# Performance work log

Measured on AMD Instinct MI355X. Metric: run time of the kernel, lower is better.

Reference implementation:

```python
import jax, jax.numpy as jnp
import numpy as np

D_MODEL = 1024
HIDDEN = 4096
N_EXPERTS = 8
TOP_K = 2


def setup_inputs() -> dict:
    key = jax.random.key(0)
    k_x, k_r, k_w1, k_w2 = jax.random.split(key, 4)
    x = jax.random.normal(k_x, (2, 1024, D_MODEL), dtype=jnp.float32)
    # router: nn.Linear(d_model, n_experts, bias=False) -> weight [E, D]; store transposed [D, E]
    Wr = jax.random.normal(k_r, (D_MODEL, N_EXPERTS), dtype=jnp.float32) * 0.02
    # expert w1: Linear(D, H) -> store [E, D, H]; w2: Linear(H, D) -> [E, H, D]
    W1 = jax.random.normal(k_w1, (N_EXPERTS, D_MODEL, HIDDEN), dtype=jnp.float32) * 0.02
    W2 = jax.random.normal(k_w2, (N_EXPERTS, HIDDEN, D_MODEL), dtype=jnp.float32) * 0.02
    return {"x": x, "Wr": Wr, "W1": W1, "W2": W2}


def reference(x, Wr, W1, W2):
    B, S, D = x.shape
    flat = x.reshape(-1, D)                       # [T, D]
    logits = flat @ Wr                            # [T, E]
    top_vals, top_idx = jax.lax.top_k(logits, TOP_K)
    # softmax over the top-k logits; forward only uses slot 0 (faithful to source)
    weights = jax.nn.softmax(top_vals, axis=-1)   # [T, K]
    top1 = top_idx[:, 0]                          # [T] int
    w_top1 = weights[:, 0]                        # [T]
    # dense all-expert compute (fixed small E loop fused into batched einsum)
    h = jax.nn.gelu(jnp.einsum('td,edh->teh', flat, W1), approximate=False)  # [T,E,H]
    y = jnp.einsum('teh,ehd->ted', h, W2)         # [T, E, D]
    y_sel = jnp.take_along_axis(y, top1[:, None, None], axis=1)[:, 0, :]     # [T, D]
    out = (w_top1[:, None] * y_sel).reshape(B, S, D)
    return out
```

## Files before the change

### kernel.cpp

```cpp
#include <hip/hip_runtime.h>
#include <math.h>

#define T_TOKENS 2048
#define DMODEL   1024
#define HID      4096
#define NEXP     8
#define MAX_TILES 32

typedef float  f32x4  __attribute__((ext_vector_type(4)));
typedef short  bf16x8 __attribute__((ext_vector_type(8)));

__device__ __forceinline__ unsigned short f2bf(float f) {
    union { float f; unsigned u; } v; v.f = f;
    unsigned u = v.u;
    unsigned r = (u + 0x7FFFu + ((u >> 16) & 1u)) >> 16;
    return (unsigned short)r;
}

__device__ __forceinline__ unsigned pk2bf(float lo, float hi) {
    unsigned r;
    asm("v_cvt_pk_bf16_f32 %0, %1, %2" : "=v"(r) : "v"(lo), "v"(hi));
    return r;
}

__device__ __forceinline__ float f4get(const float4& v, int i) {
    return i == 0 ? v.x : i == 1 ? v.y : i == 2 ? v.z : v.w;
}

__device__ __forceinline__ void async_copy16(const void* g, void* l) {
    __builtin_amdgcn_global_load_lds(
        (const __attribute__((address_space(1))) void*)g,
        (__attribute__((address_space(3))) void*)l,
        16, 0, 0);
}

__global__ __launch_bounds__(64) void router_kernel(
    const float* __restrict__ x, const float* __restrict__ Wr,
    int* counts, int* expert_of, int* slot_of, float* wt_of,
    unsigned short* __restrict__ Xbf) {
    int t = blockIdx.x;
    int lane = threadIdx.x;
    const float* xr = x + (size_t)t * DMODEL;
    unsigned short* xb = Xbf + (size_t)t * DMODEL;
    float p[NEXP];
#pragma unroll
    for (int e = 0; e < NEXP; ++e) p[e] = 0.f;
#pragma unroll
    for (int q = 0; q < 4; ++q) {
        int d = q * 256 + lane * 4;
        float4 v = *(const float4*)(xr + d);
        ushort4 b;
        b.x = f2bf(v.x); b.y = f2bf(v.y); b.z = f2bf(v.z); b.w = f2bf(v.w);
        *(ushort4*)(xb + d) = b;
#pragma unroll
        for (int j = 0; j < 4; ++j) {
            float xv = f4get(v, j);
            const float* wr = Wr + (size_t)(d + j) * NEXP;
#pragma unroll
            for (int e = 0; e < NEXP; ++e) p[e] += xv * wr[e];
        }
    }
#pragma unroll
    for (int e = 0; e < NEXP; ++e) {
        for (int off = 32; off > 0; off >>= 1)
            p[e] += __shfl_down(p[e], off, 64);
    }
    if (lane == 0) {
        int i0 = 0; float v0 = p[0];
        for (int e = 1; e < NEXP; ++e) if (p[e] > v0) { v0 = p[e]; i0 = e; }
        float v1 = -INFINITY;
        for (int e = 0; e < NEXP; ++e) if (e != i0 && p[e] > v1) v1 = p[e];
        float w = 1.f / (1.f + expf(v1 - v0));
        expert_of[t] = i0;
        wt_of[t] = w;
        slot_of[t] = atomicAdd(&counts[i0], 1);
    }
}

__global__ void scan_scatter_kernel(const int* counts, int* offsets,
                                    int* tileE, int* tileM, int* tileCount,
                                    const int* expert_of, const int* slot_of,
                                    int* perm) {
    __shared__ int soff[NEXP];
    if (threadIdx.x == 0) {
        int run = 0, tc = 0;
        for (int e = 0; e < NEXP; ++e) {
            offsets[e] = run; soff[e] = run;
            for (int m0 = 0; m0 < counts[e]; m0 += 128) {
                tileE[tc] = e; tileM[tc] = m0; ++tc;
            }
            run += counts[e];
        }
        *tileCount = tc;
    }
    __syncthreads();
    for (int t = threadIdx.x; t < T_TOKENS; t += blockDim.x)
        perm[soff[expert_of[t]] + slot_of[t]] = t;
}

__global__ __launch_bounds__(256, 2) void gemm1_kernel(
    const unsigned short* __restrict__ Xbf, const float* __restrict__ W1,
    const int* __restrict__ counts, const int* __restrict__ offsets,
    const int* __restrict__ perm, const int* __restrict__ tileE,
    const int* __restrict__ tileM, const int* __restrict__ tileCount,
    unsigned short* __restrict__ H) {

    const int NT = HID / 128;
    int tile = blockIdx.x / NT;
    int nt   = blockIdx.x % NT;
    if (tile >= *tileCount) return;
    int e = tileE[tile], m0 = tileM[tile];
    int rows_e = counts[e], base = offsets[e];
    int n0 = nt * 128;

    __shared__ unsigned short Alds[2][128 * 64];
    __shared__ unsigned short Blds[2][128 * 64];

    int tid  = threadIdx.x;
    int lane = tid & 63;
    int wid  = tid >> 6;
    int wm = wid >> 1, wn = wid & 1;
    const int swz = (lane & 7) << 4;

    const unsigned short* ag[4];
    int aoff[4];
#pragma unroll
    for (int p = 0; p < 4; ++p) {
        int idx = p * 256 + tid;
        int row = idx >> 3;
        int seg = (idx & 7) ^ (row & 7);
        int r = m0 + row;
        int tok = perm[base + (r < rows_e ? r : rows_e - 1)];
        ag[p] = Xbf + (size_t)tok * DMODEL + seg * 8;
        aoff[p] = idx * 16;
    }

    const int kq4 = (tid & 15) * 4;
    const int nb  = (tid >> 4) * 8;
    const float* bsrc = W1 + ((size_t)e * DMODEL + kq4) * HID + n0 + nb;
    float4 breg[8];

    f32x4 acc[4][4];
#pragma unroll
    for (int i = 0; i < 4; ++i)
#pragma unroll
        for (int j = 0; j < 4; ++j) acc[i][j] = (f32x4){0.f, 0.f, 0.f, 0.f};

#define G_ISSUE(kt, BUF, STRIDE) do {                                         \
    _Pragma("unroll")                                                         \
    for (int r_ = 0; r_ < 4; ++r_) {                                          \
        _Pragma("unroll")                                                     \
        for (int q_ = 0; q_ < 2; ++q_)                                        \
            breg[r_*2+q_] = *(const float4*)(bsrc + ((size_t)(kt)*64 + r_) * (STRIDE) + q_*4); \
    }                                                                         \
    _Pragma("unroll")                                                         \
    for (int p_ = 0; p_ < 4; ++p_)                                            \
        async_copy16(ag[p_] + (kt) * 64, (char*)Alds[BUF] + aoff[p_]);        \
} while (0)

#define G_WRITEB(BUF) do {                                                    \
    char* bb_ = (char*)Blds[BUF];                                             \
    _Pragma("unroll")                                                         \
    for (int j_ = 0; j_ < 8; ++j_) {                                          \
        unsigned lo_ = pk2bf(f4get(breg[0 + (j_>>2)], j_&3),                  \
                             f4get(breg[2 + (j_>>2)], j_&3));                 \
        unsigned hi_ = pk2bf(f4get(breg[4 + (j_>>2)], j_&3),                  \
                             f4get(breg[6 + (j_>>2)], j_&3));                 \
        unsigned long long w_ = ((unsigned long long)hi_ << 32) | lo_;        \
        *(unsigned long long*)(bb_ + (nb + j_) * 128 + ((kq4 * 2) ^ (j_ << 4))) = w_; \
    }                                                                         \
} while (0)

#define G_COMPUTE(BUF) do {                                                   \
    const char* ab_ = (const char*)Alds[BUF];                                 \
    const char* bb_ = (const char*)Blds[BUF];                                 \
    _Pragma("unroll")                                                         \
    for (int ks_ = 0; ks_ < 2; ++ks_) {                                       \
        int kb_ = (ks_ * 32 + ((lane >> 4) * 8)) * 2;                         \
        bf16x8 af_[4], bf_[4];                                                \
        _Pragma("unroll")                                                     \
        for (int i_ = 0; i_ < 4; ++i_) {                                      \
            int m_ = wm * 64 + i_ * 16 + (lane & 15);                         \
            af_[i_] = *(const bf16x8*)(ab_ + m_ * 128 + (kb_ ^ swz));         \
            int n_ = wn * 64 + i_ * 16 + (lane & 15);                         \
            bf_[i_] = *(const bf16x8*)(bb_ + n_ * 128 + (kb_ ^ swz));         \
        }                                                                     \
        _Pragma("unroll")                                                     \
        for (int i_ = 0; i_ < 4; ++i_)                                        \
            _Pragma("unroll")                                                 \
            for (int j_ = 0; j_ < 4; ++j_)                                    \
                acc[i_][j_] = __builtin_amdgcn_mfma_f32_16x16x32_bf16(af_[i_], bf_[j_], acc[i_][j_], 0, 0, 0); \
    }                                                                         \
} while (0)

    G_ISSUE(0, 0, HID);
    G_WRITEB(0);
    __syncthreads();

#pragma unroll 1
    for (int t = 0; t < 16; t += 2) {
        G_ISSUE(t + 1, 1, HID);
        G_COMPUTE(0);
        G_WRITEB(1);
        __syncthreads();
        if (t + 2 < 16) G_ISSUE(t + 2, 0, HID);
        G_COMPUTE(1);
        if (t + 2 < 16) G_WRITEB(0);
        __syncthreads();
    }

    int quad = lane >> 4, col = lane & 15;
#pragma unroll
    for (int i = 0; i < 4; ++i)
#pragma unroll
        for (int j = 0; j < 4; ++j)
#pragma unroll
            for (int r = 0; r < 4; ++r) {
                int ml = wm * 64 + i * 16 + quad * 4 + r;
                if (m0 + ml < rows_e) {
                    int n = n0 + wn * 64 + j * 16 + col;
                    float v = acc[i][j][r];
                    float g = 0.5f * v * (1.0f + erff(v * 0.70710678118654752f));
                    H[(size_t)(base + m0 + ml) * HID + n] = f2bf(g);
                }
            }
}

__global__ __launch_bounds__(256, 2) void gemm2_kernel(
    const unsigned short* __restrict__ H, const float* __restrict__ W2,
    const int* __restrict__ counts, const int* __restrict__ offsets,
    const int* __restrict__ perm, const float* __restrict__ wt_of,
    const int* __restrict__ tileE, const int* __restrict__ tileM,
    const int* __restrict__ tileCount, float* __restrict__ out) {

    const int NT = DMODEL / 128;
    const int SK = 4;
    int tile = blockIdx.x / (NT * SK);
    int rem  = blockIdx.x % (NT * SK);
    int nt   = rem >> 2;
    int sk   = rem & 3;
    if (tile >= *tileCount) return;
    int e = tileE[tile], m0 = tileM[tile];
    int rows_e = counts[e], base = offsets[e];
    int n0 = nt * 128;
    int kbeg = sk * (HID / SK);

    __shared__ unsigned short Alds[2][128 * 64];
    __shared__ unsigned short Blds[2][128 * 64];
    __shared__ int   rowTok[128];
    __shared__ float rowW[128];

    int tid  = threadIdx.x;
    int lane = tid & 63;
    int wid  = tid >> 6;
    int wm = wid >> 1, wn = wid & 1;
    const int swz = (lane & 7) << 4;

    if (tid < 128) {
        int r = m0 + tid;
        if (r < rows_e) {
            int tok = perm[base + r];
            rowTok[tid] = tok;
            rowW[tid]   = wt_of[tok];
        } else { rowTok[tid] = 0; rowW[tid] = 0.f; }
    }

    const unsigned short* ag[4];
    int aoff[4];
#pragma unroll
    for (int p = 0; p < 4; ++p) {
        int idx = p * 256 + tid;
        int row = idx >> 3;
        int seg = (idx & 7) ^ (row & 7);
        int hr = base + m0 + row;
        if (hr > T_TOKENS - 1) hr = T_TOKENS - 1;
        ag[p] = H + (size_t)hr * HID + kbeg + seg * 8;
        aoff[p] = idx * 16;
    }

    const int kq4 = (tid & 15) * 4;
    const int nb  = (tid >> 4) * 8;
    const float* bsrc = W2 + ((size_t)e * HID + kbeg + kq4) * DMODEL + n0 + nb;
    float4 breg[8];

    f32x4 acc[4][4];
#pragma unroll
    for (int i = 0; i < 4; ++i)
#pragma unroll
        for (int j = 0; j < 4; ++j) acc[i][j] = (f32x4){0.f, 0.f, 0.f, 0.f};

    G_ISSUE(0, 0, DMODEL);
    G_WRITEB(0);
    __syncthreads();

#pragma unroll 1
    for (int t = 0; t < 16; t += 2) {
        G_ISSUE(t + 1, 1, DMODEL);
        G_COMPUTE(0);
        G_WRITEB(1);
        __syncthreads();
        if (t + 2 < 16) G_ISSUE(t + 2, 0, DMODEL);
        G_COMPUTE(1);
        if (t + 2 < 16) G_WRITEB(0);
        __syncthreads();
    }

    int quad = lane >> 4, col = lane & 15;
#pragma unroll
    for (int i = 0; i < 4; ++i)
#pragma unroll
        for (int j = 0; j < 4; ++j)
#pragma unroll
            for (int r = 0; r < 4; ++r) {
                int ml = wm * 64 + i * 16 + quad * 4 + r;
                if (m0 + ml < rows_e) {
                    int tok = rowTok[ml];
                    float w = rowW[ml];
                    int n = n0 + wn * 64 + j * 16 + col;
                    atomicAdd(&out[(size_t)tok * DMODEL + n], w * acc[i][j][r]);
                }
            }
}

extern "C" void kernel_launch(void* const* d_in, const int* in_sizes, int n_in,
                              void* d_out, int out_size, void* d_ws, size_t ws_size,
                              hipStream_t stream) {
    const float* x  = (const float*)d_in[0];
    const float* Wr = (const float*)d_in[1];
    const float* W1 = (const float*)d_in[2];
    const float* W2 = (const float*)d_in[3];
    float* out = (float*)d_out;

    char* ws = (char*)d_ws;
    int*   counts    = (int*)(ws);
    int*   offsets   = (int*)(ws + 64);
    int*   tileCount = (int*)(ws + 128);
    int*   tileE     = (int*)(ws + 256);
    int*   tileM     = (int*)(ws + 256 + 4 * MAX_TILES);
    int*   expert_of = (int*)(ws + 1024);
    int*   slot_of   = (int*)(ws + 1024 + 8192);
    float* wt_of     = (float*)(ws + 1024 + 16384);
    int*   perm      = (int*)(ws + 1024 + 24576);
    size_t off = 65536;
    unsigned short* Xbf  = (unsigned short*)(ws + off); off += (size_t)T_TOKENS * DMODEL * 2;
    unsigned short* Hbuf = (unsigned short*)(ws + off);

    hipMemsetAsync(counts, 0, 64, stream);
    hipMemsetAsync(out, 0, (size_t)T_TOKENS * DMODEL * sizeof(float), stream);

    router_kernel<<<T_TOKENS, 64, 0, stream>>>(x, Wr, counts, expert_of, slot_of, wt_of, Xbf);
    scan_scatter_kernel<<<1, 256, 0, stream>>>(counts, offsets, tileE, tileM, tileCount,
                                               expert_of, slot_of, perm);

    gemm1_kernel<<<MAX_TILES * (HID / 128), 256, 0, stream>>>(
        Xbf, W1, counts, offsets, perm, tileE, tileM, tileCount, Hbuf);
    gemm2_kernel<<<MAX_TILES * (DMODEL / 128) * 4, 256, 0, stream>>>(
        Hbuf, W2, counts, offsets, perm, wt_of, tileE, tileM, tileCount, out);
}
```

Before: 438.2 us.

## Double threads per GEMM block and register-prefetch A/B tiles two stages ahead

```diff
diff --git a/kernel.cpp b/kernel.cpp
--- a/kernel.cpp
+++ b/kernel.cpp
@@ -27,19 +27,21 @@
     return i == 0 ? v.x : i == 1 ? v.y : i == 2 ? v.z : v.w;
 }
 
-__device__ __forceinline__ void async_copy16(const void* g, void* l) {
-    __builtin_amdgcn_global_load_lds(
-        (const __attribute__((address_space(1))) void*)g,
-        (__attribute__((address_space(3))) void*)l,
-        16, 0, 0);
-}
-
-__global__ __launch_bounds__(64) void router_kernel(
+#define SBAR() __builtin_amdgcn_sched_barrier(0)
+
+__device__ __forceinline__ void barrier_lds() {
+    asm volatile("s_waitcnt lgkmcnt(0)" ::: "memory");
+    SBAR();
+    __builtin_amdgcn_s_barrier();
+    SBAR();
+}
+
+__global__ __launch_bounds__(256) void router_kernel(
     const float* __restrict__ x, const float* __restrict__ Wr,
     int* counts, int* expert_of, int* slot_of, float* wt_of,
     unsigned short* __restrict__ Xbf) {
-    int t = blockIdx.x;
-    int lane = threadIdx.x;
+    int lane = threadIdx.x & 63;
+    int t = blockIdx.x * 4 + (threadIdx.x >> 6);
     const float* xr = x + (size_t)t * DMODEL;
     unsigned short* xb = Xbf + (size_t)t * DMODEL;
     float p[NEXP];
@@ -98,7 +100,7 @@
         perm[soff[expert_of[t]] + slot_of[t]] = t;
 }
 
-__global__ __launch_bounds__(256, 2) void gemm1_kernel(
+__global__ __launch_bounds__(512, 4) void gemm1_kernel(
     const unsigned short* __restrict__ Xbf, const float* __restrict__ W1,
     const int* __restrict__ counts, const int* __restrict__ offsets,
     const int* __restrict__ perm, const int* __restrict__ tileE,
@@ -122,101 +124,103 @@
     int wm = wid >> 1, wn = wid & 1;
     const int swz = (lane & 7) << 4;
 
-    const unsigned short* ag[4];
-    int aoff[4];
-#pragma unroll
-    for (int p = 0; p < 4; ++p) {
-        int idx = p * 256 + tid;
-        int row = idx >> 3;
-        int seg = (idx & 7) ^ (row & 7);
+    const unsigned short* ag[2];
+    int awr[2];
+#pragma unroll
+    for (int p = 0; p < 2; ++p) {
+        int idx = p * 512 + tid;
+        int row = idx >> 3, seg = idx & 7;
         int r = m0 + row;
         int tok = perm[base + (r < rows_e ? r : rows_e - 1)];
-        ag[p] = Xbf + (size_t)tok * DMODEL + seg * 8;
-        aoff[p] = idx * 16;
-    }
-
+        ag[p]  = Xbf + (size_t)tok * DMODEL + seg * 8;
+        awr[p] = row * 128 + ((seg * 16) ^ ((row & 7) << 4));
+    }
     const int kq4 = (tid & 15) * 4;
-    const int nb  = (tid >> 4) * 8;
-    const float* bsrc = W1 + ((size_t)e * DMODEL + kq4) * HID + n0 + nb;
-    float4 breg[8];
-
-    f32x4 acc[4][4];
-#pragma unroll
-    for (int i = 0; i < 4; ++i)
+    const int n4  = ((tid >> 4) & 31) * 4;
+    const float* bsrc = W1 + ((size_t)e * DMODEL + kq4) * HID + n0 + n4;
+    int bwr[4];
+#pragma unroll
+    for (int j = 0; j < 4; ++j) {
+        int n = n4 + j;
+        bwr[j] = n * 128 + ((kq4 * 2) ^ ((n & 7) << 4));
+    }
+
+    f32x4 acc[2][4];
+#pragma unroll
+    for (int i = 0; i < 2; ++i)
 #pragma unroll
         for (int j = 0; j < 4; ++j) acc[i][j] = (f32x4){0.f, 0.f, 0.f, 0.f};
 
-#define G_ISSUE(kt, BUF, STRIDE) do {                                         \
+    float4 areg[2]; float4 breg[4];
+
+#define G_LOADA(kt) do {                                                      \
+    areg[0] = *(const float4*)(ag[0] + (kt) * 64);                            \
+    areg[1] = *(const float4*)(ag[1] + (kt) * 64);                            \
+} while (0)
+#define G_LOADB(kt, STRIDE) do {                                              \
     _Pragma("unroll")                                                         \
-    for (int r_ = 0; r_ < 4; ++r_) {                                          \
-        _Pragma("unroll")                                                     \
-        for (int q_ = 0; q_ < 2; ++q_)                                        \
-            breg[r_*2+q_] = *(const float4*)(bsrc + ((size_t)(kt)*64 + r_) * (STRIDE) + q_*4); \
-    }                                                                         \
+    for (int r_ = 0; r_ < 4; ++r_)                                            \
+        breg[r_] = *(const float4*)(bsrc + ((size_t)(kt) * 64 + r_) * (STRIDE)); \
+} while (0)
+#define G_STAGE(BUF) do {                                                     \
+    *(float4*)((char*)Alds[BUF] + awr[0]) = areg[0];                          \
+    *(float4*)((char*)Alds[BUF] + awr[1]) = areg[1];                          \
     _Pragma("unroll")                                                         \
-    for (int p_ = 0; p_ < 4; ++p_)                                            \
-        async_copy16(ag[p_] + (kt) * 64, (char*)Alds[BUF] + aoff[p_]);        \
-} while (0)
-
-#define G_WRITEB(BUF) do {                                                    \
-    char* bb_ = (char*)Blds[BUF];                                             \
-    _Pragma("unroll")                                                         \
-    for (int j_ = 0; j_ < 8; ++j_) {                                          \
-        unsigned lo_ = pk2bf(f4get(breg[0 + (j_>>2)], j_&3),                  \
-                             f4get(breg[2 + (j_>>2)], j_&3));                 \
-        unsigned hi_ = pk2bf(f4get(breg[4 + (j_>>2)], j_&3),                  \
-                             f4get(breg[6 + (j_>>2)], j_&3));                 \
+    for (int j_ = 0; j_ < 4; ++j_) {                                          \
+        unsigned lo_ = pk2bf(f4get(breg[0], j_), f4get(breg[1], j_));         \
+        unsigned hi_ = pk2bf(f4get(breg[2], j_), f4get(breg[3], j_));         \
         unsigned long long w_ = ((unsigned long long)hi_ << 32) | lo_;        \
-        *(unsigned long long*)(bb_ + (nb + j_) * 128 + ((kq4 * 2) ^ (j_ << 4))) = w_; \
+        *(unsigned long long*)((char*)Blds[BUF] + bwr[j_]) = w_;              \
     }                                                                         \
 } while (0)
-
 #define G_COMPUTE(BUF) do {                                                   \
     const char* ab_ = (const char*)Alds[BUF];                                 \
     const char* bb_ = (const char*)Blds[BUF];                                 \
     _Pragma("unroll")                                                         \
     for (int ks_ = 0; ks_ < 2; ++ks_) {                                       \
         int kb_ = (ks_ * 32 + ((lane >> 4) * 8)) * 2;                         \
-        bf16x8 af_[4], bf_[4];                                                \
+        bf16x8 af_[2], bf_[4];                                                \
         _Pragma("unroll")                                                     \
-        for (int i_ = 0; i_ < 4; ++i_) {                                      \
-            int m_ = wm * 64 + i_ * 16 + (lane & 15);                         \
+        for (int i_ = 0; i_ < 2; ++i_) {                                      \
+            int m_ = wm * 32 + i_ * 16 + (lane & 15);                         \
             af_[i_] = *(const bf16x8*)(ab_ + m_ * 128 + (kb_ ^ swz));         \
-            int n_ = wn * 64 + i_ * 16 + (lane & 15);                         \
-            bf_[i_] = *(const bf16x8*)(bb_ + n_ * 128 + (kb_ ^ swz));         \
         }                                                                     \
         _Pragma("unroll")                                                     \
-        for (int i_ = 0; i_ < 4; ++i_)                                        \
+        for (int j_ = 0; j_ < 4; ++j_) {                                      \
+            int n_ = wn * 64 + j_ * 16 + (lane & 15);                         \
+            bf_[j_] = *(const bf16x8*)(bb_ + n_ * 128 + (kb_ ^ swz));         \
+        }                                                                     \
+        _Pragma("unroll")                                                     \
+        for (int i_ = 0; i_ < 2; ++i_)                                        \
             _Pragma("unroll")                                                 \
             for (int j_ = 0; j_ < 4; ++j_)                                    \
                 acc[i_][j_] = __builtin_amdgcn_mfma_f32_16x16x32_bf16(af_[i_], bf_[j_], acc[i_][j_], 0, 0, 0); \
     }                                                                         \
 } while (0)
 
-    G_ISSUE(0, 0, HID);
-    G_WRITEB(0);
-    __syncthreads();
+    G_LOADA(0); G_LOADB(0, HID);
+    G_STAGE(0);
+    G_LOADA(1); G_LOADB(1, HID);
+    barrier_lds();
 
 #pragma unroll 1
-    for (int t = 0; t < 16; t += 2) {
-        G_ISSUE(t + 1, 1, HID);
-        G_COMPUTE(0);
-        G_WRITEB(1);
-        __syncthreads();
-        if (t + 2 < 16) G_ISSUE(t + 2, 0, HID);
-        G_COMPUTE(1);
-        if (t + 2 < 16) G_WRITEB(0);
-        __syncthreads();
-    }
+    for (int t = 0; t < 15; ++t) {
+        int cur = t & 1, nxt = cur ^ 1;
+        G_STAGE(nxt);
+        G_COMPUTE(cur);
+        if (t < 14) { G_LOADA(t + 2); G_LOADB(t + 2, HID); }
+        barrier_lds();
+    }
+    G_COMPUTE(1);
 
     int quad = lane >> 4, col = lane & 15;
 #pragma unroll
-    for (int i = 0; i < 4; ++i)
+    for (int i = 0; i < 2; ++i)
 #pragma unroll
         for (int j = 0; j < 4; ++j)
 #pragma unroll
             for (int r = 0; r < 4; ++r) {
-                int ml = wm * 64 + i * 16 + quad * 4 + r;
+                int ml = wm * 32 + i * 16 + quad * 4 + r;
                 if (m0 + ml < rows_e) {
                     int n = n0 + wn * 64 + j * 16 + col;
                     float v = acc[i][j][r];
@@ -226,7 +230,7 @@
             }
 }
 
-__global__ __launch_bounds__(256, 2) void gemm2_kernel(
+__global__ __launch_bounds__(512, 4) void gemm2_kernel(
     const unsigned short* __restrict__ H, const float* __restrict__ W2,
     const int* __restrict__ counts, const int* __restrict__ offsets,
     const int* __restrict__ perm, const float* __restrict__ wt_of,
@@ -234,16 +238,15 @@
     const int* __restrict__ tileCount, float* __restrict__ out) {
 
     const int NT = DMODEL / 128;
-    const int SK = 4;
-    int tile = blockIdx.x / (NT * SK);
-    int rem  = blockIdx.x % (NT * SK);
+    int tile = blockIdx.x / (NT * 4);
+    int rem  = blockIdx.x % (NT * 4);
     int nt   = rem >> 2;
     int sk   = rem & 3;
     if (tile >= *tileCount) return;
     int e = tileE[tile], m0 = tileM[tile];
     int rows_e = counts[e], base = offsets[e];
     int n0 = nt * 128;
-    int kbeg = sk * (HID / SK);
+    int kbeg = sk * (HID / 4);
 
     __shared__ unsigned short Alds[2][128 * 64];
     __shared__ unsigned short Blds[2][128 * 64];
@@ -265,54 +268,58 @@
         } else { rowTok[tid] = 0; rowW[tid] = 0.f; }
     }
 
-    const unsigned short* ag[4];
-    int aoff[4];
-#pragma unroll
-    for (int p = 0; p < 4; ++p) {
-        int idx = p * 256 + tid;
-        int row = idx >> 3;
-        int seg = (idx & 7) ^ (row & 7);
+    const unsigned short* ag[2];
+    int awr[2];
+#pragma unroll
+    for (int p = 0; p < 2; ++p) {
+        int idx = p * 512 + tid;
+        int row = idx >> 3, seg = idx & 7;
         int hr = base + m0 + row;
         if (hr > T_TOKENS - 1) hr = T_TOKENS - 1;
-        ag[p] = H + (size_t)hr * HID + kbeg + seg * 8;
-        aoff[p] = idx * 16;
-    }
-
+        ag[p]  = H + (size_t)hr * HID + kbeg + seg * 8;
+        awr[p] = row * 128 + ((seg * 16) ^ ((row & 7) << 4));
+    }
     const int kq4 = (tid & 15) * 4;
-    const int nb  = (tid >> 4) * 8;
-    const float* bsrc = W2 + ((size_t)e * HID + kbeg + kq4) * DMODEL + n0 + nb;
-    float4 breg[8];
-
-    f32x4 acc[4][4];
-#pragma unroll
-    for (int i = 0; i < 4; ++i)
+    const int n4  = ((tid >> 4) & 31) * 4;
+    const float* bsrc = W2 + ((size_t)e * HID + kbeg + kq4) * DMODEL + n0 + n4;
+    int bwr[4];
+#pragma unroll
+    for (int j = 0; j < 4; ++j) {
+        int n = n4 + j;
+        bwr[j] = n * 128 + ((kq4 * 2) ^ ((n & 7) << 4));
+    }
+
+    f32x4 acc[2][4];
+#pragma unroll
+    for (int i = 0; i < 2; ++i)
 #pragma unroll
         for (int j = 0; j < 4; ++j) acc[i][j] = (f32x4){0.f, 0.f, 0.f, 0.f};
 
-    G_ISSUE(0, 0, DMODEL);
-    G_WRITEB(0);
-    __syncthreads();
+    float4 areg[2]; float4 breg[4];
+
+    G_LOADA(0); G_LOADB(0, DMODEL);
+    G_STAGE(0);
+    G_LOADA(1); G_LOADB(1, DMODEL);
+    barrier_lds();
 
 #pragma unroll 1
-    for (int t = 0; t < 16; t += 2) {
-        G_ISSUE(t + 1, 1, DMODEL);
-        G_COMPUTE(0);
-        G_WRITEB(1);
-        __syncthreads();
-        if (t + 2 < 16) G_ISSUE(t + 2, 0, DMODEL);
-        G_COMPUTE(1);
-        if (t + 2 < 16) G_WRITEB(0);
-        __syncthreads();
-    }
+    for (int t = 0; t < 15; ++t) {
+        int cur = t & 1, nxt = cur ^ 1;
+        G_STAGE(nxt);
+        G_COMPUTE(cur);
+        if (t < 14) { G_LOADA(t + 2); G_LOADB(t + 2, DMODEL); }
+        barrier_lds();
+    }
+    G_COMPUTE(1);
 
     int quad = lane >> 4, col = lane & 15;
 #pragma unroll
-    for (int i = 0; i < 4; ++i)
+    for (int i = 0; i < 2; ++i)
 #pragma unroll
         for (int j = 0; j < 4; ++j)
 #pragma unroll
             for (int r = 0; r < 4; ++r) {
-                int ml = wm * 64 + i * 16 + quad * 4 + r;
+                int ml = wm * 32 + i * 16 + quad * 4 + r;
                 if (m0 + ml < rows_e) {
                     int tok = rowTok[ml];
                     float w = rowW[ml];
@@ -348,12 +355,12 @@
     hipMemsetAsync(counts, 0, 64, stream);
     hipMemsetAsync(out, 0, (size_t)T_TOKENS * DMODEL * sizeof(float), stream);
 
-    router_kernel<<<T_TOKENS, 64, 0, stream>>>(x, Wr, counts, expert_of, slot_of, wt_of, Xbf);
+    router_kernel<<<T_TOKENS / 4, 256, 0, stream>>>(x, Wr, counts, expert_of, slot_of, wt_of, Xbf);
     scan_scatter_kernel<<<1, 256, 0, stream>>>(counts, offsets, tileE, tileM, tileCount,
                                                expert_of, slot_of, perm);
 
-    gemm1_kernel<<<MAX_TILES * (HID / 128), 256, 0, stream>>>(
+    gemm1_kernel<<<MAX_TILES * (HID / 128), 512, 0, stream>>>(
         Xbf, W1, counts, offsets, perm, tileE, tileM, tileCount, Hbuf);
-    gemm2_kernel<<<MAX_TILES * (DMODEL / 128) * 4, 256, 0, stream>>>(
+    gemm2_kernel<<<MAX_TILES * (DMODEL / 128) * 4, 512, 0, stream>>>(
         Hbuf, W2, counts, offsets, perm, wt_of, tileE, tileM, tileCount, out);
 }
```

Result: slower. 465.7 us (+6.3%).
